# Kernel tuning notes

Measured on AMD Instinct MI355X. Metric: run time of the kernel, lower is better.

## Reference

```python
import jax, jax.numpy as jnp
import numpy as np

B, T, N_EMBED, HEAD_SIZE = 8, 2048, 1024, 64


def setup_inputs() -> dict:
    key = jax.random.key(0)
    kx, kq, kk, kv = jax.random.split(key, 4)
    x = jax.random.normal(kx, (B, T, N_EMBED), dtype=jnp.float32)
    # nn.Linear(n_embed, head_size, bias=False) -> weight [head_size, n_embed];
    # we store the transposed [n_embed, head_size] so projection is x @ W.
    s = 1.0 / np.sqrt(N_EMBED)
    Wq = jax.random.normal(kq, (N_EMBED, HEAD_SIZE), dtype=jnp.float32) * s
    Wk = jax.random.normal(kk, (N_EMBED, HEAD_SIZE), dtype=jnp.float32) * s
    Wv = jax.random.normal(kv, (N_EMBED, HEAD_SIZE), dtype=jnp.float32) * s
    pad_mask = jnp.ones((B, T), dtype=jnp.int32)
    return {"x": x, "pad_mask": pad_mask, "Wq": Wq, "Wk": Wk, "Wv": Wv}


def reference(x, pad_mask, Wq, Wk, Wv):
    Bq, Tq, C = x.shape  # C == n_embed
    q = x @ Wq  # [B,T,H]
    k = x @ Wk  # self-attention path (enc_x is None)
    v = x @ Wv
    # NOTE: original divides by C**0.5 with C = n_embed, not head_size.
    scores = jnp.einsum("bth,bsh->bts", q, k) / jnp.sqrt(jnp.asarray(C, x.dtype))
    causal = jnp.tril(jnp.ones((Tq, Tq), dtype=bool))  # tril[:T,:T] != 0
    keep = causal[None, :, :] & (pad_mask[:, None, :] != 0)  # [B,T,T]
    scores = jnp.where(keep, scores, -jnp.inf)
    attn = jax.nn.softmax(scores, axis=-1)
    return jnp.einsum("bts,bsh->bth", attn, v)  # [B,T,head_size]
```

## Files before the change

kernel.cpp:

```cpp
#include <hip/hip_runtime.h>

#define DEV static __device__ __forceinline__

typedef float f32x4 __attribute__((ext_vector_type(4)));
typedef int i32x4 __attribute__((ext_vector_type(4)));
typedef __bf16 bf16x8 __attribute__((ext_vector_type(8)));
typedef unsigned short u16x8 __attribute__((ext_vector_type(8)));
typedef unsigned short u16x4 __attribute__((ext_vector_type(4)));

#define MFMA(a, b, c) __builtin_amdgcn_mfma_f32_16x16x32_bf16((a), (b), (c), 0, 0, 0)

#define WAIT8_BARRIER() asm volatile("s_waitcnt vmcnt(8)\n\ts_barrier" ::: "memory")
#define LGKM_BARRIER()  asm volatile("s_waitcnt lgkmcnt(0)\n\ts_barrier" ::: "memory")
#define VM_DRAIN()      asm volatile("s_waitcnt vmcnt(0)" ::: "memory")

#define TT 2048
#define CE 1024
#define HS 64

#define WBT_E 0
#define Q_E   196608
#define K_E   (Q_E + 1048576)
#define VT_E  (K_E + 1048576)
#define PO_E  (VT_E + 1048576)
#define PML_E (PO_E + 2097152)

DEV unsigned short cvt_bf16(float f) {
    unsigned int u = __builtin_bit_cast(unsigned int, f);
    u += 0x7FFFu + ((u >> 16) & 1u);
    return (unsigned short)(u >> 16);
}

DEV float bf2f(unsigned short v) {
    unsigned int u = ((unsigned int)v) << 16;
    return __builtin_bit_cast(float, u);
}

DEV bf16x8 ld_bf8(const unsigned short* p) {
    union { u16x8 u; bf16x8 b; } v;
    v.u = *(const u16x8*)p;
    return v.b;
}

DEV bf16x8 as_bf8(u16x8 u) {
    union { u16x8 u; bf16x8 b; } v;
    v.u = u;
    return v.b;
}

DEV void glds16(const void* g, void* l) {
    __builtin_amdgcn_global_load_lds(
        (const __attribute__((address_space(1))) void*)g,
        (__attribute__((address_space(3))) void*)l, 16, 0, 0);
}

__global__ __launch_bounds__(256) void wconv_kernel(
        const float* __restrict__ Wq, const float* __restrict__ Wk,
        const float* __restrict__ Wv, unsigned short* __restrict__ wbt) {
    __shared__ unsigned short Tr[64 * 72];
    const int blk = blockIdx.x;
    const int head = blk >> 4, kt = blk & 15;
    const int k0 = kt * 64;
    const float* W = (head == 0) ? Wq : ((head == 1) ? Wk : Wv);
    const float sc = (head == 0) ? 0.045084220027780106f : 1.0f;
    const int t = threadIdx.x;
    const int rrow = t >> 4, c4 = (t & 15) * 4;
    for (int i = 0; i < 4; ++i) {
        int krow = rrow + i * 16;
        f32x4 f = *(const f32x4*)(W + (size_t)(k0 + krow) * 64 + c4);
        Tr[(c4 + 0) * 72 + krow] = cvt_bf16(f[0] * sc);
        Tr[(c4 + 1) * 72 + krow] = cvt_bf16(f[1] * sc);
        Tr[(c4 + 2) * 72 + krow] = cvt_bf16(f[2] * sc);
        Tr[(c4 + 3) * 72 + krow] = cvt_bf16(f[3] * sc);
    }
    __syncthreads();
    const int n = t >> 2, off = (t & 3) * 16;
    u16x8 a0 = *(const u16x8*)&Tr[n * 72 + off];
    u16x8 a1 = *(const u16x8*)&Tr[n * 72 + off + 8];
    unsigned short* dst = wbt + head * 65536 + n * 1024 + k0 + off;
    *(u16x8*)dst = a0;
    *(u16x8*)(dst + 8) = a1;
}

__global__ __launch_bounds__(256) void proj_kernel(
        const float* __restrict__ x, const unsigned short* __restrict__ wbt,
        unsigned short* __restrict__ qws, unsigned short* __restrict__ kws,
        unsigned short* __restrict__ vtws) {
    __shared__ __align__(16) float Xt0[1024], Xt1[1024], Xt2[1024], Xt3[1024];
    __shared__ __align__(16) unsigned short Wt0[6144], Wt1[6144], Wt2[6144], Wt3[6144];
    __shared__ __align__(16) unsigned short TT2[64 * 48];

    const int t = threadIdx.x;
    const int lane = t & 63, w = t >> 6;
    const int quad = lane >> 4, c = lane & 15;
    const int wm = w & 1, wn = w >> 1;
    const int t0 = blockIdx.x * 32;

    const int srow = lane >> 3, scb = (lane & 7) ^ srow;
    const float* xg = x + (size_t)(t0 + w * 8 + srow) * CE + scb * 4;
    const int wrow_lo = lane >> 2;
    const int wcb = (lane & 3) ^ (wrow_lo & 3);
    const unsigned short* wg0 = wbt + (size_t)((3 * w + 0) * 16 + wrow_lo) * 1024 + wcb * 8;
    const unsigned short* wg1 = wbt + (size_t)((3 * w + 1) * 16 + wrow_lo) * 1024 + wcb * 8;
    const unsigned short* wg2 = wbt + (size_t)((3 * w + 2) * 16 + wrow_lo) * 1024 + wcb * 8;

#define PSTAGE(XD, WD, ksn) \
    glds16(xg + (ksn), &XD[w * 256]); \
    glds16(wg0 + (ksn), &WD[(3 * w + 0) * 512]); \
    glds16(wg1 + (ksn), &WD[(3 * w + 1) * 512]); \
    glds16(wg2 + (ksn), &WD[(3 * w + 2) * 512]);

    f32x4 acc[6] = {};

    PSTAGE(Xt0, Wt0, 0)
    PSTAGE(Xt1, Wt1, 32)
    PSTAGE(Xt2, Wt2, 64)

    const int r = wm * 16 + c;
    const int ck7 = c & 7, ck3 = c & 3;

#define PITER(step, XT, WT, XD, WD) { \
    WAIT8_BARRIER(); \
    f32x4 v0 = *(const f32x4*)&XT[r * 32 + (((2 * quad) ^ ck7) * 4)]; \
    f32x4 v1 = *(const f32x4*)&XT[r * 32 + (((2 * quad + 1) ^ ck7) * 4)]; \
    u16x8 ap; \
    _Pragma("unroll") for (int j = 0; j < 4; ++j) { \
        ap[j] = cvt_bf16(v0[j]); ap[4 + j] = cvt_bf16(v1[j]); } \
    bf16x8 af = as_bf8(ap); \
    _Pragma("unroll") for (int nt = 0; nt < 6; ++nt) { \
        bf16x8 bb = ld_bf8(&WT[(wn * 96 + nt * 16 + c) * 32 + ((quad ^ ck3) * 8)]); \
        acc[nt] = MFMA(af, bb, acc[nt]); } \
    const int ksn = (((step) + 3) & 31) * 32; \
    PSTAGE(XD, WD, ksn) }

    for (int s = 0; s < 32; s += 4) {
        PITER(s + 0, Xt0, Wt0, Xt3, Wt3)
        PITER(s + 1, Xt1, Wt1, Xt0, Wt0)
        PITER(s + 2, Xt2, Wt2, Xt1, Wt1)
        PITER(s + 3, Xt3, Wt3, Xt2, Wt2)
    }
#undef PITER
#undef PSTAGE

    for (int nt = 0; nt < 6; ++nt) {
        int col = wn * 96 + nt * 16 + c;
        f32x4 a = acc[nt];
        for (int r4 = 0; r4 < 4; ++r4) {
            int row = wm * 16 + quad * 4 + r4;
            size_t tg = (size_t)(t0 + row);
            unsigned short hv = cvt_bf16(a[r4]);
            if (col < 64)       qws[tg * HS + col] = hv;
            else if (col < 128) kws[tg * HS + col - 64] = hv;
            else                TT2[(col - 128) * 48 + row] = hv;
        }
    }
    __syncthreads();
    {
        int h = t >> 2, off = (t & 3) * 8;
        u16x8 v = *(const u16x8*)&TT2[h * 48 + off];
        int b = t0 >> 11, tl0 = t0 & 2047;
        *(u16x8*)(vtws + (size_t)(b * 64 + h) * TT + tl0 + off) = v;
    }
}

__global__ __launch_bounds__(256) void flash_kernel(
        const unsigned short* __restrict__ qws, const unsigned short* __restrict__ kws,
        const unsigned short* __restrict__ vtws, const int* __restrict__ pmask,
        unsigned short* __restrict__ pO, float* __restrict__ pml) {
    __shared__ __align__(16) unsigned short Kt0[4096], Kt1[4096], Kt2[4096], Kt3[4096];
    __shared__ __align__(16) unsigned short Vt0[4096], Vt1[4096], Vt2[4096], Vt3[4096];
    __shared__ __align__(16) unsigned short Ps[4][1152];
    __shared__ __align__(16) float Bs[1024];

    const int t = threadIdx.x, blk = blockIdx.x;
    const int sp = blk >> 8, r8 = blk & 255, b = r8 & 7;
    int qt = r8 >> 3;
    if (sp) qt = 31 - qt;
    if (sp && qt == 0) return;
    const int half = (qt + 2) >> 1;
    const int jbeg = sp ? half : 0;
    const int jend = sp ? qt + 1 : half;
    const int niter = jend - jbeg;

    const int lane = t & 63, w = t >> 6;
    const int quad = lane >> 4, c = lane & 15;

    const int srow = lane >> 3, scb = (lane & 7) ^ srow;
    const unsigned short* kg0 = kws + (size_t)(b * TT + 2 * w * 8 + srow) * HS + scb * 8;
    const unsigned short* kg1 = kg0 + (size_t)8 * HS;
    const unsigned short* vg0 = vtws + (size_t)(b * 64 + 2 * w * 8 + srow) * TT + scb * 8;
    const unsigned short* vg1 = vg0 + (size_t)8 * TT;

#define FSTAGE(KD, VD, kv) \
    glds16(kg0 + (size_t)(kv) * HS, &KD[(2 * w + 0) * 512]); \
    glds16(kg1 + (size_t)(kv) * HS, &KD[(2 * w + 1) * 512]); \
    glds16(vg0 + (kv), &VD[(2 * w + 0) * 512]); \
    glds16(vg1 + (kv), &VD[(2 * w + 1) * 512]);

    bf16x8 qf[2];
#pragma unroll
    for (int kk = 0; kk < 2; ++kk)
        qf[kk] = ld_bf8(qws + (size_t)(b * TT + qt * 64 + w * 16 + c) * HS + kk * 32 + quad * 8);

    {
        int bi = t * 4;
        if (bi < niter * 64) {
            i32x4 pmv = *(const i32x4*)(pmask + b * TT + jbeg * 64 + bi);
            f32x4 bvv;
#pragma unroll
            for (int j = 0; j < 4; ++j) bvv[j] = pmv[j] ? 0.0f : -1e30f;
            *(f32x4*)&Bs[bi] = bvv;
        }
    }

    {
        int j1 = (jbeg + 1 > jend - 1) ? jend - 1 : jbeg + 1;
        int j2 = (jbeg + 2 > jend - 1) ? jend - 1 : jbeg + 2;
        FSTAGE(Kt0, Vt0, jbeg * 64)
        FSTAGE(Kt1, Vt1, j1 * 64)
        FSTAGE(Kt2, Vt2, j2 * 64)
    }
    LGKM_BARRIER();

    f32x4 o[4] = {};
    float m_run = -1e30f, l_run = 0.0f;
    const int ck7 = c & 7;

#define FITER(u, KT, VT, KD, VD) \
    if (j0 + (u) < jend) { \
        const int j = j0 + (u); \
        WAIT8_BARRIER(); \
        f32x4 bv[4]; \
        _Pragma("unroll") for (int nt = 0; nt < 4; ++nt) \
            bv[nt] = *(const f32x4*)&Bs[(j - jbeg) * 64 + nt * 16 + quad * 4]; \
        f32x4 s4[4] = {}; \
        _Pragma("unroll") for (int kk = 0; kk < 2; ++kk) \
        _Pragma("unroll") for (int nt = 0; nt < 4; ++nt) { \
            bf16x8 ka = ld_bf8(&KT[(nt * 16 + c) * 64 + (((kk * 4 + quad) ^ ck7) * 8)]); \
            s4[nt] = MFMA(ka, qf[kk], s4[nt]); } \
        if (j == qt) { \
            const int qrl = w * 16 + c; \
            _Pragma("unroll") for (int nt = 0; nt < 4; ++nt) \
            _Pragma("unroll") for (int r = 0; r < 4; ++r) { \
                int kvl = nt * 16 + quad * 4 + r; \
                s4[nt][r] = (kvl > qrl) ? -1e30f : (s4[nt][r] + bv[nt][r]); } \
        } else { \
            _Pragma("unroll") for (int nt = 0; nt < 4; ++nt) \
            _Pragma("unroll") for (int r = 0; r < 4; ++r) s4[nt][r] += bv[nt][r]; } \
        float mx = s4[0][0]; \
        _Pragma("unroll") for (int nt = 0; nt < 4; ++nt) \
        _Pragma("unroll") for (int r = 0; r < 4; ++r) mx = fmaxf(mx, s4[nt][r]); \
        mx = fmaxf(mx, __shfl_xor(mx, 16, 64)); \
        mx = fmaxf(mx, __shfl_xor(mx, 32, 64)); \
        float mnew = fmaxf(m_run, mx); \
        float al = exp2f(m_run - mnew); \
        m_run = mnew; \
        _Pragma("unroll") for (int nt = 0; nt < 4; ++nt) \
        _Pragma("unroll") for (int r = 0; r < 4; ++r) s4[nt][r] = exp2f(s4[nt][r] - mnew); \
        float rs = 0.0f; \
        _Pragma("unroll") for (int nt = 0; nt < 4; ++nt) \
            rs += (s4[nt][0] + s4[nt][1]) + (s4[nt][2] + s4[nt][3]); \
        rs += __shfl_xor(rs, 16, 64); \
        rs += __shfl_xor(rs, 32, 64); \
        l_run = l_run * al + rs; \
        _Pragma("unroll") for (int ht = 0; ht < 4; ++ht) \
        _Pragma("unroll") for (int r = 0; r < 4; ++r) o[ht][r] *= al; \
        _Pragma("unroll") for (int nt = 0; nt < 4; ++nt) { \
            u16x4 pk; \
            _Pragma("unroll") for (int r = 0; r < 4; ++r) pk[r] = cvt_bf16(s4[nt][r]); \
            *(u16x4*)&Ps[w][c * 72 + nt * 16 + quad * 4] = pk; } \
        bf16x8 p0 = ld_bf8(&Ps[w][c * 72 + quad * 8]); \
        bf16x8 p1 = ld_bf8(&Ps[w][c * 72 + 32 + quad * 8]); \
        _Pragma("unroll") for (int kk = 0; kk < 2; ++kk) { \
            bf16x8 pa = kk ? p1 : p0; \
            _Pragma("unroll") for (int ht = 0; ht < 4; ++ht) { \
                bf16x8 va = ld_bf8(&VT[(ht * 16 + c) * 64 + (((kk * 4 + quad) ^ ck7) * 8)]); \
                o[ht] = MFMA(va, pa, o[ht]); } } \
        int jn = j + 3; if (jn > jend - 1) jn = jend - 1; \
        FSTAGE(KD, VD, jn * 64) \
    }

    for (int j0 = jbeg; j0 < jend; j0 += 4) {
        FITER(0, Kt0, Vt0, Kt3, Vt3)
        FITER(1, Kt1, Vt1, Kt0, Vt0)
        FITER(2, Kt2, Vt2, Kt1, Vt1)
        FITER(3, Kt3, Vt3, Kt2, Vt2)
    }
#undef FITER
#undef FSTAGE

    VM_DRAIN();

    unsigned short* po = pO + (size_t)blk * 4096;
#pragma unroll
    for (int ht = 0; ht < 4; ++ht) {
        u16x4 pk;
#pragma unroll
        for (int r = 0; r < 4; ++r) pk[r] = cvt_bf16(o[ht][r]);
        *(u16x4*)(po + (w * 16 + c) * 64 + ht * 16 + quad * 4) = pk;
    }
    if (quad == 0) {
        pml[(size_t)blk * 128 + (w * 16 + c) * 2] = m_run;
        pml[(size_t)blk * 128 + (w * 16 + c) * 2 + 1] = l_run;
    }
}

__global__ __launch_bounds__(256) void combine_kernel(
        const unsigned short* __restrict__ pO, const float* __restrict__ pml,
        float* __restrict__ out) {
    const int blk = blockIdx.x;
    const int qt = blk >> 3, b = blk & 7;
    const int s0 = qt * 8 + b, s1 = 256 + (31 - qt) * 8 + b;
    const bool two = (qt > 0);
    const int t = threadIdx.x, h = t & 63, rg = t >> 6;
    for (int i = 0; i < 16; ++i) {
        int row = rg + i * 4;
        float m0 = pml[(size_t)s0 * 128 + row * 2];
        float l0 = pml[(size_t)s0 * 128 + row * 2 + 1];
        float o0 = bf2f(pO[(size_t)s0 * 4096 + row * 64 + h]);
        float num, den;
        if (two) {
            float m1 = pml[(size_t)s1 * 128 + row * 2];
            float l1 = pml[(size_t)s1 * 128 + row * 2 + 1];
            float o1 = bf2f(pO[(size_t)s1 * 4096 + row * 64 + h]);
            float M = fmaxf(m0, m1);
            float w0 = exp2f(m0 - M), w1 = exp2f(m1 - M);
            num = o0 * w0 + o1 * w1;
            den = l0 * w0 + l1 * w1;
        } else {
            num = o0; den = l0;
        }
        out[(size_t)(b * TT + qt * 64 + row) * HS + h] = num / den;
    }
}

extern "C" void kernel_launch(void* const* d_in, const int* in_sizes, int n_in,
                              void* d_out, int out_size, void* d_ws, size_t ws_size,
                              hipStream_t stream) {
    const float* x  = (const float*)d_in[0];
    const int* pm   = (const int*)d_in[1];
    const float* Wq = (const float*)d_in[2];
    const float* Wk = (const float*)d_in[3];
    const float* Wv = (const float*)d_in[4];
    float* out = (float*)d_out;

    unsigned short* wsu  = (unsigned short*)d_ws;
    unsigned short* wbt  = wsu + WBT_E;
    unsigned short* qws  = wsu + Q_E;
    unsigned short* kws  = wsu + K_E;
    unsigned short* vtws = wsu + VT_E;
    unsigned short* pO   = wsu + PO_E;
    float* pml           = (float*)(wsu + PML_E);

    wconv_kernel<<<48, 256, 0, stream>>>(Wq, Wk, Wv, wbt);
    proj_kernel<<<512, 256, 0, stream>>>(x, wbt, qws, kws, vtws);
    flash_kernel<<<512, 256, 0, stream>>>(qws, kws, vtws, pm, pO, pml);
    combine_kernel<<<256, 256, 0, stream>>>(pO, pml, out);
}
```

Measured before the change: 158.1 us.

## Load projection operands directly from global into registers, dropping LDS staging

The projection kernel no longer stages x and the weights through a 4-deep LDS ring with global_load_lds and barriers. Each wave now loads its MFMA fragments straight from global memory into registers, double-buffered in software, and converts x to bf16 with native casts. The warp tiling also changes so that each wave owns 48 output columns across both 16-row tiles, which lets one B fragment feed two MFMAs. This removes the LDS traffic and the per-step barriers, at the cost of more VGPRs and less coalesced global loads.

After: 178.3 us. 12.8% more time.

```diff
diff --git a/kernel.cpp b/kernel.cpp
--- a/kernel.cpp
+++ b/kernel.cpp
@@ -46,6 +46,16 @@
     union { u16x8 u; bf16x8 b; } v;
     v.u = u;
     return v.b;
+}
+
+DEV bf16x8 cvt8(f32x4 a, f32x4 b) {
+    bf16x8 r;
+#pragma unroll
+    for (int j = 0; j < 4; ++j) {
+        r[j] = (__bf16)a[j];
+        r[4 + j] = (__bf16)b[j];
+    }
+    return r;
 }
 
 DEV void glds16(const void* g, void* l) {
@@ -86,72 +96,80 @@
         const float* __restrict__ x, const unsigned short* __restrict__ wbt,
         unsigned short* __restrict__ qws, unsigned short* __restrict__ kws,
         unsigned short* __restrict__ vtws) {
-    __shared__ __align__(16) float Xt0[1024], Xt1[1024], Xt2[1024], Xt3[1024];
-    __shared__ __align__(16) unsigned short Wt0[6144], Wt1[6144], Wt2[6144], Wt3[6144];
     __shared__ __align__(16) unsigned short TT2[64 * 48];
 
     const int t = threadIdx.x;
     const int lane = t & 63, w = t >> 6;
     const int quad = lane >> 4, c = lane & 15;
-    const int wm = w & 1, wn = w >> 1;
     const int t0 = blockIdx.x * 32;
 
-    const int srow = lane >> 3, scb = (lane & 7) ^ srow;
-    const float* xg = x + (size_t)(t0 + w * 8 + srow) * CE + scb * 4;
-    const int wrow_lo = lane >> 2;
-    const int wcb = (lane & 3) ^ (wrow_lo & 3);
-    const unsigned short* wg0 = wbt + (size_t)((3 * w + 0) * 16 + wrow_lo) * 1024 + wcb * 8;
-    const unsigned short* wg1 = wbt + (size_t)((3 * w + 1) * 16 + wrow_lo) * 1024 + wcb * 8;
-    const unsigned short* wg2 = wbt + (size_t)((3 * w + 2) * 16 + wrow_lo) * 1024 + wcb * 8;
-
-#define PSTAGE(XD, WD, ksn) \
-    glds16(xg + (ksn), &XD[w * 256]); \
-    glds16(wg0 + (ksn), &WD[(3 * w + 0) * 512]); \
-    glds16(wg1 + (ksn), &WD[(3 * w + 1) * 512]); \
-    glds16(wg2 + (ksn), &WD[(3 * w + 2) * 512]);
-
-    f32x4 acc[6] = {};
-
-    PSTAGE(Xt0, Wt0, 0)
-    PSTAGE(Xt1, Wt1, 32)
-    PSTAGE(Xt2, Wt2, 64)
-
-    const int r = wm * 16 + c;
-    const int ck7 = c & 7, ck3 = c & 3;
-
-#define PITER(step, XT, WT, XD, WD) { \
-    WAIT8_BARRIER(); \
-    f32x4 v0 = *(const f32x4*)&XT[r * 32 + (((2 * quad) ^ ck7) * 4)]; \
-    f32x4 v1 = *(const f32x4*)&XT[r * 32 + (((2 * quad + 1) ^ ck7) * 4)]; \
-    u16x8 ap; \
-    _Pragma("unroll") for (int j = 0; j < 4; ++j) { \
-        ap[j] = cvt_bf16(v0[j]); ap[4 + j] = cvt_bf16(v1[j]); } \
-    bf16x8 af = as_bf8(ap); \
-    _Pragma("unroll") for (int nt = 0; nt < 6; ++nt) { \
-        bf16x8 bb = ld_bf8(&WT[(wn * 96 + nt * 16 + c) * 32 + ((quad ^ ck3) * 8)]); \
-        acc[nt] = MFMA(af, bb, acc[nt]); } \
-    const int ksn = (((step) + 3) & 31) * 32; \
-    PSTAGE(XD, WD, ksn) }
-
-    for (int s = 0; s < 32; s += 4) {
-        PITER(s + 0, Xt0, Wt0, Xt3, Wt3)
-        PITER(s + 1, Xt1, Wt1, Xt0, Wt0)
-        PITER(s + 2, Xt2, Wt2, Xt1, Wt1)
-        PITER(s + 3, Xt3, Wt3, Xt2, Wt2)
-    }
-#undef PITER
-#undef PSTAGE
-
-    for (int nt = 0; nt < 6; ++nt) {
-        int col = wn * 96 + nt * 16 + c;
-        f32x4 a = acc[nt];
-        for (int r4 = 0; r4 < 4; ++r4) {
-            int row = wm * 16 + quad * 4 + r4;
-            size_t tg = (size_t)(t0 + row);
-            unsigned short hv = cvt_bf16(a[r4]);
-            if (col < 64)       qws[tg * HS + col] = hv;
-            else if (col < 128) kws[tg * HS + col - 64] = hv;
-            else                TT2[(col - 128) * 48 + row] = hv;
+    const float* xg0 = x + (size_t)(t0 + c) * CE + quad * 8;
+    const float* xg1 = xg0 + (size_t)16 * CE;
+    const unsigned short* wg0 = wbt + (size_t)(w * 48 + c) * CE + quad * 8;
+    const unsigned short* wg1 = wg0 + (size_t)16 * CE;
+    const unsigned short* wg2 = wg0 + (size_t)32 * CE;
+
+    f32x4 acc[2][3] = {};
+
+    f32x4 xa[2][2][2], xb[2][2][2];
+    u16x8 wa[3][2], wb[3][2];
+
+#define LOADX(XS) { \
+    _Pragma("unroll") for (int kk = 0; kk < 2; ++kk) { \
+        XS[0][kk][0] = *(const f32x4*)(xg0 + kk * 32); \
+        XS[0][kk][1] = *(const f32x4*)(xg0 + kk * 32 + 4); \
+        XS[1][kk][0] = *(const f32x4*)(xg1 + kk * 32); \
+        XS[1][kk][1] = *(const f32x4*)(xg1 + kk * 32 + 4); } }
+
+#define LOADW(WS) { \
+    _Pragma("unroll") for (int kk = 0; kk < 2; ++kk) { \
+        WS[0][kk] = *(const u16x8*)(wg0 + kk * 32); \
+        WS[1][kk] = *(const u16x8*)(wg1 + kk * 32); \
+        WS[2][kk] = *(const u16x8*)(wg2 + kk * 32); } }
+
+#define ADV() { xg0 += 64; xg1 += 64; wg0 += 64; wg1 += 64; wg2 += 64; }
+
+#define COMPUTE(XS, WS) { \
+    _Pragma("unroll") for (int kk = 0; kk < 2; ++kk) { \
+        bf16x8 af0 = cvt8(XS[0][kk][0], XS[0][kk][1]); \
+        bf16x8 af1 = cvt8(XS[1][kk][0], XS[1][kk][1]); \
+        _Pragma("unroll") for (int nt = 0; nt < 3; ++nt) { \
+            bf16x8 bbf = as_bf8(WS[nt][kk]); \
+            acc[0][nt] = MFMA(af0, bbf, acc[0][nt]); \
+            acc[1][nt] = MFMA(af1, bbf, acc[1][nt]); } } }
+
+    LOADX(xa) LOADW(wa) ADV()
+
+    for (int i = 0; i < 14; i += 2) {
+        LOADX(xb) LOADW(wb) ADV()
+        COMPUTE(xa, wa)
+        LOADX(xa) LOADW(wa) ADV()
+        COMPUTE(xb, wb)
+    }
+    LOADX(xb) LOADW(wb)
+    COMPUTE(xa, wa)
+    COMPUTE(xb, wb)
+
+#undef LOADX
+#undef LOADW
+#undef ADV
+#undef COMPUTE
+
+#pragma unroll
+    for (int am = 0; am < 2; ++am) {
+#pragma unroll
+        for (int nt = 0; nt < 3; ++nt) {
+            int col = w * 48 + nt * 16 + c;
+            f32x4 a = acc[am][nt];
+#pragma unroll
+            for (int r4 = 0; r4 < 4; ++r4) {
+                int row = am * 16 + quad * 4 + r4;
+                size_t tg = (size_t)(t0 + row);
+                unsigned short hv = cvt_bf16(a[r4]);
+                if (col < 64)       qws[tg * HS + col] = hv;
+                else if (col < 128) kws[tg * HS + col - 64] = hv;
+                else                TT2[(col - 128) * 48 + row] = hv;
+            }
         }
     }
     __syncthreads();
```

## Double projection kernel threads to 512 and split output tiles per wave

Applied to the files above, without the earlier changes.

The QKV projection kernel now runs 8 waves per block instead of 4. Each wave computes 3 of the 16-wide output column tiles instead of 6. The global-to-LDS staging is redistributed: two waves load the X tile and six waves load the weight tile, each issuing 2 loads per stage, so the wait count drops to vmcnt(4). The aim is more latency hiding and MFMA parallelism in the projection. The cost is more barrier participants, and per-wave load work is now uneven.

Result: slower. 162.0 us (+2.5%).

```diff
diff --git a/kernel.cpp b/kernel.cpp
--- a/kernel.cpp
+++ b/kernel.cpp
@@ -11,6 +11,7 @@
 #define MFMA(a, b, c) __builtin_amdgcn_mfma_f32_16x16x32_bf16((a), (b), (c), 0, 0, 0)
 
 #define WAIT8_BARRIER() asm volatile("s_waitcnt vmcnt(8)\n\ts_barrier" ::: "memory")
+#define WAIT4_BARRIER() asm volatile("s_waitcnt vmcnt(4)\n\ts_barrier" ::: "memory")
 #define LGKM_BARRIER()  asm volatile("s_waitcnt lgkmcnt(0)\n\ts_barrier" ::: "memory")
 #define VM_DRAIN()      asm volatile("s_waitcnt vmcnt(0)" ::: "memory")
 
@@ -82,7 +83,7 @@
     *(u16x8*)(dst + 8) = a1;
 }
 
-__global__ __launch_bounds__(256) void proj_kernel(
+__global__ __launch_bounds__(512, 4) void proj_kernel(
         const float* __restrict__ x, const unsigned short* __restrict__ wbt,
         unsigned short* __restrict__ qws, unsigned short* __restrict__ kws,
         unsigned short* __restrict__ vtws) {
@@ -97,38 +98,42 @@
     const int t0 = blockIdx.x * 32;
 
     const int srow = lane >> 3, scb = (lane & 7) ^ srow;
-    const float* xg = x + (size_t)(t0 + w * 8 + srow) * CE + scb * 4;
-    const int wrow_lo = lane >> 2;
-    const int wcb = (lane & 3) ^ (wrow_lo & 3);
-    const unsigned short* wg0 = wbt + (size_t)((3 * w + 0) * 16 + wrow_lo) * 1024 + wcb * 8;
-    const unsigned short* wg1 = wbt + (size_t)((3 * w + 1) * 16 + wrow_lo) * 1024 + wcb * 8;
-    const unsigned short* wg2 = wbt + (size_t)((3 * w + 2) * 16 + wrow_lo) * 1024 + wcb * 8;
+    const int wrow = lane >> 2, wcb = (lane & 3) ^ (wrow & 3);
+    const int xrow = (w < 2) ? (t0 + w * 16 + srow) : t0;
+    const int wbase = (w < 2) ? 0 : (w - 2) * 32;
+    const float* xg0 = x + (size_t)xrow * CE + scb * 4;
+    const float* xg1 = xg0 + (size_t)8 * CE;
+    const unsigned short* wg0 = wbt + (size_t)(wbase + wrow) * 1024 + wcb * 8;
+    const unsigned short* wg1 = wg0 + (size_t)16 * 1024;
 
 #define PSTAGE(XD, WD, ksn) \
-    glds16(xg + (ksn), &XD[w * 256]); \
-    glds16(wg0 + (ksn), &WD[(3 * w + 0) * 512]); \
-    glds16(wg1 + (ksn), &WD[(3 * w + 1) * 512]); \
-    glds16(wg2 + (ksn), &WD[(3 * w + 2) * 512]);
-
-    f32x4 acc[6] = {};
+    if (w < 2) { \
+        glds16(xg0 + (ksn), &XD[w * 512]); \
+        glds16(xg1 + (ksn), &XD[w * 512 + 256]); \
+    } else { \
+        glds16(wg0 + (ksn), &WD[wbase * 32]); \
+        glds16(wg1 + (ksn), &WD[wbase * 32 + 512]); \
+    }
+
+    f32x4 acc[3] = {};
 
     PSTAGE(Xt0, Wt0, 0)
     PSTAGE(Xt1, Wt1, 32)
     PSTAGE(Xt2, Wt2, 64)
 
-    const int r = wm * 16 + c;
+    const int r32 = (wm * 16 + c) * 32;
     const int ck7 = c & 7, ck3 = c & 3;
 
 #define PITER(step, XT, WT, XD, WD) { \
-    WAIT8_BARRIER(); \
-    f32x4 v0 = *(const f32x4*)&XT[r * 32 + (((2 * quad) ^ ck7) * 4)]; \
-    f32x4 v1 = *(const f32x4*)&XT[r * 32 + (((2 * quad + 1) ^ ck7) * 4)]; \
+    WAIT4_BARRIER(); \
+    f32x4 v0 = *(const f32x4*)&XT[r32 + (((2 * quad) ^ ck7) * 4)]; \
+    f32x4 v1 = *(const f32x4*)&XT[r32 + (((2 * quad + 1) ^ ck7) * 4)]; \
     u16x8 ap; \
     _Pragma("unroll") for (int j = 0; j < 4; ++j) { \
         ap[j] = cvt_bf16(v0[j]); ap[4 + j] = cvt_bf16(v1[j]); } \
     bf16x8 af = as_bf8(ap); \
-    _Pragma("unroll") for (int nt = 0; nt < 6; ++nt) { \
-        bf16x8 bb = ld_bf8(&WT[(wn * 96 + nt * 16 + c) * 32 + ((quad ^ ck3) * 8)]); \
+    _Pragma("unroll") for (int nt = 0; nt < 3; ++nt) { \
+        bf16x8 bb = ld_bf8(&WT[(wn * 48 + nt * 16 + c) * 32 + ((quad ^ ck3) * 8)]); \
         acc[nt] = MFMA(af, bb, acc[nt]); } \
     const int ksn = (((step) + 3) & 31) * 32; \
     PSTAGE(XD, WD, ksn) }
@@ -142,9 +147,11 @@
 #undef PITER
 #undef PSTAGE
 
-    for (int nt = 0; nt < 6; ++nt) {
-        int col = wn * 96 + nt * 16 + c;
+#pragma unroll
+    for (int nt = 0; nt < 3; ++nt) {
+        int col = wn * 48 + nt * 16 + c;
         f32x4 a = acc[nt];
+#pragma unroll
         for (int r4 = 0; r4 < 4; ++r4) {
             int row = wm * 16 + quad * 4 + r4;
             size_t tg = (size_t)(t0 + row);
@@ -155,7 +162,7 @@
         }
     }
     __syncthreads();
-    {
+    if (t < 256) {
         int h = t >> 2, off = (t & 3) * 8;
         u16x8 v = *(const u16x8*)&TT2[h * 48 + off];
         int b = t0 >> 11, tl0 = t0 & 2047;
@@ -353,7 +360,7 @@
     float* pml           = (float*)(wsu + PML_E);
 
     wconv_kernel<<<48, 256, 0, stream>>>(Wq, Wk, Wv, wbt);
-    proj_kernel<<<512, 256, 0, stream>>>(x, wbt, qws, kws, vtws);
+    proj_kernel<<<512, 512, 0, stream>>>(x, wbt, qws, kws, vtws);
     flash_kernel<<<512, 256, 0, stream>>>(qws, kws, vtws, pm, pO, pml);
     combine_kernel<<<256, 256, 0, stream>>>(pO, pml, out);
 }
```
